# Performance work log

Measured on AMD Instinct MI355X. Metric: run time of the kernel, lower is better.

## Reference

```python
import jax, jax.numpy as jnp
import numpy as np

N_NODES = 2048
N_EDGES = 32768
DIM = 256
HEADS = 4

PARAM_SHAPES = {
    'Wq': (DIM, DIM), 'bq': (DIM,), 'Wk': (DIM, DIM), 'bk': (DIM,),
    'Wv': (DIM, DIM), 'bv': (DIM,), 'Wo': (DIM, DIM), 'bo': (DIM,),
    'gd_W1': (4, 3), 'gd_b1': (3,), 'gd_W2': (3, HEADS), 'gd_b2': (HEADS,),
    'tw_W1': (2 * DIM, DIM), 'tw_b1': (DIM,), 'tw_W2': (DIM, DIM), 'tw_b2': (DIM,),
    'ne_W1': (4 * DIM, 2 * DIM), 'ne_b1': (2 * DIM,), 'ne_W2': (2 * DIM, DIM), 'ne_b2': (DIM,),
    'att_W1': (2 * DIM // HEADS, 2 * DIM // HEADS), 'att_b1': (2 * DIM // HEADS,),
    'att_W2': (DIM // HEADS, 2 * DIM // HEADS), 'att_b2': (DIM // HEADS,),
    'pe_W': (DIM, DIM), 'pe_b': (DIM,), 'pq_W': (DIM, DIM), 'pq_b': (DIM,),
    'pv_W': (DIM, DIM), 'pv_b': (DIM,),
    'pr_W1': (2 * DIM, 2 * DIM), 'pr_b1': (2 * DIM,), 'pr_W2': (2 * DIM, DIM), 'pr_b2': (DIM,),
}


def _lin(x, W, b):
    return x @ W + b


def _mlp2(x, W1, b1, W2, b2):  # Linear-ReLU-Linear (build_mlp, on_last=False)
    return _lin(jnp.maximum(_lin(x, W1, b1), 0.0), W2, b2)


def setup_inputs() -> dict:
    key = jax.random.key(0)
    ks = iter(jax.random.split(key, 64))
    rng = np.random.default_rng(0)
    half = N_EDGES // 2
    s = rng.integers(0, N_NODES, half)
    d = rng.integers(0, N_NODES, half)
    # reciprocal edge pairs so the reverse-edge lookup path is exercised
    edge_index = jnp.asarray(np.stack([np.concatenate([s, d]), np.concatenate([d, s])]), dtype=jnp.int32)
    inp = {
        'node_f': jax.random.normal(next(ks), (N_NODES, DIM), jnp.float32),
        'edge_f': jax.random.normal(next(ks), (N_EDGES, DIM), jnp.float32),
        'coords': jax.random.normal(next(ks), (N_NODES, 3), jnp.float32),
        'edge_index': edge_index,
        'num_heads': HEADS,
    }
    for name, shp in PARAM_SHAPES.items():
        inp[name] = jax.random.normal(next(ks), shp, jnp.float32) * 0.02
    return inp


def _forward(node_f, edge_f, coords, edge_index, num_heads,
             Wq, bq, Wk, bk, Wv, bv, Wo, bo,
             gd_W1, gd_b1, gd_W2, gd_b2,
             tw_W1, tw_b1, tw_W2, tw_b2,
             ne_W1, ne_b1, ne_W2, ne_b2,
             att_W1, att_b1, att_W2, att_b2,
             pe_W, pe_b, pq_W, pq_b, pv_W, pv_b,
             pr_W1, pr_b1, pr_W2, pr_b2):
    N, Dn = node_f.shape
    E, De = edge_f.shape
    H = num_heads
    dh = Wq.shape[1] // H
    src, dst = edge_index[0], edge_index[1]

    # --- NodeUpdate: distance-aware MHSA over all node pairs (batch=1) ---
    q = _lin(node_f, Wq, bq).reshape(N, H, dh)
    k = _lin(node_f, Wk, bk).reshape(N, H, dh)
    v = _lin(node_f, Wv, bv).reshape(N, H, dh)
    diff = coords[:, None, :] - coords[None, :, :]  # [N,N,3]
    sq = jnp.sum(diff * diff, axis=-1, keepdims=True)
    dist = jnp.where(sq > 0, jnp.sqrt(jnp.where(sq > 0, sq, 1.0)), 0.0)
    dmask = _mlp2(jnp.concatenate([diff, dist], -1), gd_W1, gd_b1, gd_W2, gd_b2)  # [N,N,H]
    scores = jnp.einsum('nhd,mhd->hnm', q, k) / float(dh) ** 0.5 + dmask.transpose(2, 0, 1)
    attn = jax.nn.softmax(scores, axis=-1)
    mhsa = _lin(jnp.einsum('hnm,mhd->nhd', attn, v).reshape(N, H * dh), Wo, bo)

    # --- TwinningEdgeAttention: per-node mean of outgoing / incoming edge feats ---
    ones = jnp.ones((E,), edge_f.dtype)
    cnt_s = jnp.maximum(jax.ops.segment_sum(ones, src, num_segments=N), 1.0)
    cnt_d = jnp.maximum(jax.ops.segment_sum(ones, dst, num_segments=N), 1.0)
    sub_mean = jax.ops.segment_sum(edge_f, src, num_segments=N) / cnt_s[:, None]
    obj_mean = jax.ops.segment_sum(edge_f, dst, num_segments=N) / cnt_d[:, None]
    edge_att = jax.nn.sigmoid(_mlp2(jnp.concatenate([sub_mean, obj_mean], -1), tw_W1, tw_b1, tw_W2, tw_b2))
    node_out = jnp.maximum(mhsa, 0.0) * edge_att  # [N, Dn]

    # --- GraphEdgeAttenNetwork ---
    x_i = node_f[src]
    x_j = node_f[dst]
    # reverse-edge matching (vectorized replacement of the python double loop)
    table = jnp.zeros((N * N,), jnp.int32).at[src * N + dst].set(jnp.arange(E, dtype=jnp.int32) + 1)
    rev = table[dst * N + src]
    rev_feat = jnp.where((rev > 0)[:, None], edge_f[jnp.maximum(rev - 1, 0)], 0.0)
    edge_out = _mlp2(jnp.concatenate([x_i, edge_f, rev_feat, x_j], -1), ne_W1, ne_b1, ne_W2, ne_b2)

    value = _lin(x_j, pv_W, pv_b)  # [E, Da]
    query = _lin(x_i, pq_W, pq_b).reshape(E, Dn // H, H)
    edgep = _lin(edge_f, pe_W, pe_b).reshape(E, De // H, H)
    qe = jnp.concatenate([query, edgep], axis=1)  # [E, d_n+d_e, H]
    # conv1d(kernel=1) MLP over channel axis, ReLU between layers
    h = jnp.maximum(jnp.einsum('ech,oc->eoh', qe, att_W1) + att_b1[None, :, None], 0.0)
    prob = jax.nn.softmax(jnp.einsum('ech,oc->eoh', h, att_W2) + att_b2[None, :, None], axis=1)  # [E, d_o, H]
    msg = prob.reshape(E, -1) * value
    agg = jax.ops.segment_max(msg, src, num_segments=N)
    agg = jnp.where(jnp.isfinite(agg), agg, 0.0)  # empty segments -> 0 (torch scatter_max fill)
    xx = _mlp2(jnp.concatenate([node_f, agg], -1), pr_W1, pr_b1, pr_W2, pr_b2)
    return node_out, edge_out, xx


def reference(node_f, edge_f, coords, edge_index, num_heads,
              Wq, bq, Wk, bk, Wv, bv, Wo, bo,
              gd_W1, gd_b1, gd_W2, gd_b2,
              tw_W1, tw_b1, tw_W2, tw_b2,
              ne_W1, ne_b1, ne_W2, ne_b2,
              att_W1, att_b1, att_W2, att_b2,
              pe_W, pe_b, pq_W, pq_b, pv_W, pv_b,
              pr_W1, pr_b1, pr_W2, pr_b2):
    return _forward(node_f, edge_f, coords, edge_index, num_heads,
                    Wq, bq, Wk, bk, Wv, bv, Wo, bo,
                    gd_W1, gd_b1, gd_W2, gd_b2,
                    tw_W1, tw_b1, tw_W2, tw_b2,
                    ne_W1, ne_b1, ne_W2, ne_b2,
                    att_W1, att_b1, att_W2, att_b2,
                    pe_W, pe_b, pq_W, pq_b, pv_W, pv_b,
                    pr_W1, pr_b1, pr_W2, pr_b2)
```

## Files before the change

kernel.cpp:

```cpp
#include <hip/hip_runtime.h>

#define NN 2048
#define NE 32768
#define DIM 256
#define NH 4

typedef unsigned short u16;
typedef __attribute__((ext_vector_type(4))) unsigned short u16x4;
typedef __attribute__((ext_vector_type(8))) short bf16x8;
typedef __attribute__((ext_vector_type(4))) float f32x4;

typedef __attribute__((address_space(1))) const unsigned int g_as1;
typedef __attribute__((address_space(3))) unsigned int l_as3;

__device__ __forceinline__ void gload16(const u16* g, u16* l) {
  __builtin_amdgcn_global_load_lds((g_as1*)g, (l_as3*)l, 16, 0, 0);
}

__device__ __forceinline__ u16 f2bf(float f) {
  unsigned u = __float_as_uint(f);
  unsigned r = u + 0x7FFFu + ((u >> 16) & 1u);
  return (u16)(r >> 16);
}
__device__ __forceinline__ float bf2f(u16 b) {
  return __uint_as_float(((unsigned)b) << 16);
}

struct GB { const u16* A; const int* idx; long ld; long aoffz; };

template<int BNF, int EPI>
__global__ __launch_bounds__(256) void gemm_bf(
    GB ga, const u16* __restrict__ Bt, long bld, long boffz,
    const float* __restrict__ bias, void* __restrict__ Cp, long ldc, long coffz,
    int K, float scale, const float* __restrict__ extra)
{
  __shared__ u16 As[128 * 64];
  __shared__ u16 Bs[32 * BNF * 64];

  const int tid = threadIdx.x;
  const int wid = tid >> 6, lane = tid & 63;
  const int bz = blockIdx.z;
  const int m0 = blockIdx.y * 128;
  const int n0 = blockIdx.x * (32 * BNF);
  const int wr = wid >> 1, wc = wid & 1;
  const int l15 = lane & 15, l4 = lane >> 4;

  const u16* asrc[4];
  #pragma unroll
  for (int c = 0; c < 4; ++c) {
    int rl = c*32 + wid*8 + (lane >> 3);
    int row = ga.idx ? ga.idx[m0 + rl] : (m0 + rl);
    int c16s = (lane & 7) ^ (rl & 7);
    asrc[c] = ga.A + ga.aoffz * bz + (long)row * ga.ld + c16s * 8;
  }
  const u16* bsrc[BNF];
  #pragma unroll
  for (int c = 0; c < BNF; ++c) {
    int rl = c*32 + wid*8 + (lane >> 3);
    int c16s = (lane & 7) ^ (rl & 7);
    bsrc[c] = Bt + boffz * bz + (long)(n0 + rl) * bld + c16s * 8;
  }

  f32x4 acc[4][BNF] = {};

  for (int k0 = 0; k0 < K; k0 += 64) {
    #pragma unroll
    for (int c = 0; c < 4; ++c)
      gload16(asrc[c] + k0, &As[(c*32 + wid*8) * 64]);
    #pragma unroll
    for (int c = 0; c < BNF; ++c)
      gload16(bsrc[c] + k0, &Bs[(c*32 + wid*8) * 64]);
    __syncthreads();

    #pragma unroll
    for (int kk = 0; kk < 2; ++kk) {
      bf16x8 af[4], bfr[BNF];
      #pragma unroll
      for (int i = 0; i < 4; ++i) {
        int r = wr*64 + i*16 + l15;
        af[i] = *(const bf16x8*)&As[r*64 + (((kk*4 + l4) ^ (r & 7)) * 8)];
      }
      #pragma unroll
      for (int j = 0; j < BNF; ++j) {
        int r = wc*(16*BNF) + j*16 + l15;
        bfr[j] = *(const bf16x8*)&Bs[r*64 + (((kk*4 + l4) ^ (r & 7)) * 8)];
      }
      #pragma unroll
      for (int i = 0; i < 4; ++i)
        #pragma unroll
        for (int j = 0; j < BNF; ++j)
          acc[i][j] = __builtin_amdgcn_mfma_f32_16x16x32_bf16(af[i], bfr[j], acc[i][j], 0, 0, 0);
    }
    __syncthreads();
  }

  #pragma unroll
  for (int j = 0; j < BNF; ++j) {
    const int col = n0 + wc*(16*BNF) + j*16 + l15;
    const float bb = bias ? bias[col] : 0.f;
    #pragma unroll
    for (int i = 0; i < 4; ++i) {
      #pragma unroll
      for (int r = 0; r < 4; ++r) {
        const int m = m0 + wr*64 + i*16 + l4*4 + r;
        float v = acc[i][j][r] * scale + bb;
        if constexpr (EPI == 1) v = fmaxf(v, 0.f);
        if constexpr (EPI == 2) v = 1.f / (1.f + expf(-v));
        if constexpr (EPI == 9) {
          v = fmaxf(v, 0.f) * extra[(long)m*ldc + col];
          ((float*)Cp)[(long)m*ldc + col] = v;
        }
        else if constexpr (EPI == 0 || EPI == 2)
          ((float*)Cp)[coffz*bz + (long)m*ldc + col] = v;
        else if constexpr (EPI == 4)
          ((u16*)Cp)[((long)(col & 3) * NE + m) * ldc + (col >> 2) + coffz] = f2bf(v);
        else if constexpr (EPI == 8) {
          if (col < 256)
            ((float*)Cp)[(long)m*256 + (col & 3)*64 + (col >> 2)] = v;
          else {
            u16* qb = (u16*)((float*)Cp + (long)NN*256);
            int c2 = col - 256;
            qb[((long)(c2 & 3)*NN + m)*64 + (c2 >> 2)] = f2bf(v);
          }
        }
        else
          ((u16*)Cp)[coffz*bz + (long)m*ldc + col] = f2bf(v);
      }
    }
  }
}

__global__ __launch_bounds__(256) void flash_k(
    const u16* __restrict__ qkv,
    const u16* __restrict__ vT,
    const float4* __restrict__ pk,
    const float* __restrict__ gW1, const float* __restrict__ gb1,
    const float* __restrict__ gW2, const float* __restrict__ gb2,
    u16* __restrict__ Op,
    float2* __restrict__ ml)
{
  __shared__ u16 Kls[128*64];
  __shared__ u16 Vls[2][64*64];
  __shared__ u16 Pls[4][16*128];

  const int tid = threadIdx.x, wid = tid >> 6, lane = tid & 63;
  const int h  = blockIdx.x & 3;
  const int m0 = (blockIdx.x >> 2) * 64;
  const int part = blockIdx.y;
  const int l15 = lane & 15, l4 = lane >> 4;
  const int rl8 = wid*8 + (lane >> 3);
  const int c8  = lane & 7;

  bf16x8 qf[2];
  {
    const u16* qp = qkv + (long)(m0 + wid*16 + l15)*768 + h*64 + l4*8;
    qf[0] = *(const bf16x8*)(qp);
    qf[1] = *(const bf16x8*)(qp + 32);
  }

  const float b10 = gb1[0], b11 = gb1[1], b12 = gb1[2];
  const float w30 = gW1[9], w31 = gW1[10], w32 = gW1[11];
  const float w20 = gW2[0*4+h], w21 = gW2[1*4+h], w22 = gW2[2*4+h];
  const float b2h = gb2[h];
  float4 rp0[4], rp1[4];
  #pragma unroll
  for (int r = 0; r < 4; ++r) {
    int qrow = m0 + wid*16 + l4*4 + r;
    rp0[r] = pk[qrow*2]; rp1[r] = pk[qrow*2 + 1];
  }

  f32x4 pa[4] = {};
  const int n0 = part*128;

  #pragma unroll
  for (int c = 0; c < 4; ++c) {
    int r = c*32 + rl8;
    gload16(qkv + (long)(n0 + r)*768 + 256 + h*64 + ((c8 ^ (r & 7))*8),
            &Kls[(c*32 + wid*8)*64]);
  }
  #pragma unroll
  for (int hh = 0; hh < 2; ++hh)
    #pragma unroll
    for (int c = 0; c < 2; ++c) {
      int r = c*32 + rl8;
      gload16(vT + (long)(h*64 + r)*NN + n0 + hh*64 + ((c8 ^ (r & 7))*8),
              &Vls[hh][(c*32 + wid*8)*64]);
    }
  __syncthreads();

  f32x4 sa[8] = {};
  #pragma unroll
  for (int kk = 0; kk < 2; ++kk) {
    #pragma unroll
    for (int j = 0; j < 8; ++j) {
      int r = j*16 + l15;
      bf16x8 bf = *(const bf16x8*)&Kls[r*64 + (((kk*4 + l4) ^ (r & 7))*8)];
      sa[j] = __builtin_amdgcn_mfma_f32_16x16x32_bf16(qf[kk], bf, sa[j], 0, 0, 0);
    }
  }

  float rowmx[4] = {-1e30f, -1e30f, -1e30f, -1e30f};
  #pragma unroll
  for (int j = 0; j < 8; ++j) {
    int n = n0 + j*16 + l15;
    float4 cp0 = pk[n*2], cp1 = pk[n*2 + 1];
    #pragma unroll
    for (int r = 0; r < 4; ++r) {
      float dot = rp0[r].x*cp0.x + rp0[r].y*cp0.y + rp0[r].z*cp0.z;
      float sq = rp0[r].w + cp0.w - 2.f*dot;
      float dist = sq > 0.f ? sq * __frsqrt_rn(sq) : 0.f;
      float h0 = fmaxf(b10 + rp1[r].x - cp1.x + dist*w30, 0.f);
      float h1 = fmaxf(b11 + rp1[r].y - cp1.y + dist*w31, 0.f);
      float h2 = fmaxf(b12 + rp1[r].z - cp1.z + dist*w32, 0.f);
      float s = sa[j][r]*0.125f + b2h + h0*w20 + h1*w21 + h2*w22;
      sa[j][r] = s;
      rowmx[r] = fmaxf(rowmx[r], s);
    }
  }
  #pragma unroll
  for (int w = 1; w < 16; w <<= 1)
    #pragma unroll
    for (int r = 0; r < 4; ++r)
      rowmx[r] = fmaxf(rowmx[r], __shfl_xor(rowmx[r], w));

  float rs[4] = {};
  #pragma unroll
  for (int j = 0; j < 8; ++j)
    #pragma unroll
    for (int r = 0; r < 4; ++r) {
      float p = __expf(sa[j][r] - rowmx[r]);
      sa[j][r] = p;
      rs[r] += p;
    }
  #pragma unroll
  for (int w = 1; w < 16; w <<= 1)
    #pragma unroll
    for (int r = 0; r < 4; ++r)
      rs[r] += __shfl_xor(rs[r], w);

  #pragma unroll
  for (int j = 0; j < 8; ++j)
    #pragma unroll
    for (int r = 0; r < 4; ++r) {
      int qr = l4*4 + r, n = j*16 + l15;
      Pls[wid][qr*128 + (((n >> 3) ^ (qr & 7))*8) + (n & 7)] = f2bf(sa[j][r]);
    }
  asm volatile("" ::: "memory");
  #pragma unroll
  for (int ks = 0; ks < 4; ++ks) {
    bf16x8 paf = *(const bf16x8*)&Pls[wid][l15*128 + (((ks*4 + l4) ^ (l15 & 7))*8)];
    #pragma unroll
    for (int j2 = 0; j2 < 4; ++j2) {
      int r = j2*16 + l15;
      bf16x8 vf = *(const bf16x8*)&Vls[ks >> 1][r*64 + ((((ks & 1)*4 + l4) ^ (r & 7))*8)];
      pa[j2] = __builtin_amdgcn_mfma_f32_16x16x32_bf16(paf, vf, pa[j2], 0, 0, 0);
    }
  }

  #pragma unroll
  for (int j2 = 0; j2 < 4; ++j2)
    #pragma unroll
    for (int r = 0; r < 4; ++r) {
      int m = m0 + wid*16 + l4*4 + r;
      Op[((long)part*NN + m)*256 + h*64 + j2*16 + l15] = f2bf(pa[j2][r]);
    }
  if (l15 == 0) {
    #pragma unroll
    for (int r = 0; r < 4; ++r) {
      int m = m0 + wid*16 + l4*4 + r;
      ml[((long)part*NN + m)*4 + h] = make_float2(rowmx[r], rs[r]);
    }
  }
}

__global__ __launch_bounds__(256) void comb_k(const u16* __restrict__ Op,
    const float2* __restrict__ ml, u16* __restrict__ attn) {
  int n = blockIdx.x, t = threadIdx.x, h = t >> 6;
  float m[16], l[16];
  #pragma unroll
  for (int p = 0; p < 16; ++p) { float2 v = ml[((long)p*NN + n)*4 + h]; m[p] = v.x; l[p] = v.y; }
  float M = m[0];
  #pragma unroll
  for (int p = 1; p < 16; ++p) M = fmaxf(M, m[p]);
  float L = 0.f, o = 0.f;
  #pragma unroll
  for (int p = 0; p < 16; ++p) {
    float w = __expf(m[p] - M);
    L += w * l[p];
    o += w * bf2f(Op[((long)p*NN + n)*256 + t]);
  }
  attn[(long)n*256 + t] = f2bf(o / L);
}

__global__ __launch_bounds__(64) void attedge_k(
    const u16* __restrict__ qN, const u16* __restrict__ ep,
    const float* __restrict__ valNp, const int* __restrict__ ei,
    const u16* __restrict__ W1, const float* __restrict__ b1,
    const u16* __restrict__ W2, const float* __restrict__ b2,
    u16* __restrict__ msgP)
{
  __shared__ u16 As[32*128];
  const int lane = threadIdx.x;
  const int h = blockIdx.y;
  const int e0 = blockIdx.x * 32;
  const int l15 = lane & 15, l4 = lane >> 4;

  #pragma unroll
  for (int p = 0; p < 8; ++p) {
    int R0 = p*4;
    int r  = R0 + (lane >> 4);
    int cd = lane & 15;
    int cs = ((cd & 7) ^ (r & 7)) | (cd & 8);
    const u16* src = (cs < 8)
        ? qN + ((long)h*NN + ei[e0 + r])*64 + cs*8
        : ep + ((long)h*NE + e0 + r)*64 + (cs & 7)*8;
    gload16(src, &As[R0*128]);
  }
  __syncthreads();

  f32x4 acc1[2][8] = {};
  #pragma unroll
  for (int kk = 0; kk < 4; ++kk) {
    bf16x8 af[2], bfr[8];
    #pragma unroll
    for (int i = 0; i < 2; ++i) {
      int rA = i*16 + l15;
      int cg = kk*4 + l4;
      int cd = ((cg & 7) ^ (rA & 7)) | (cg & 8);
      af[i] = *(const bf16x8*)&As[rA*128 + cd*8];
    }
    #pragma unroll
    for (int j = 0; j < 8; ++j)
      bfr[j] = *(const bf16x8*)&W1[(long)(j*16 + l15)*128 + kk*32 + l4*8];
    #pragma unroll
    for (int i = 0; i < 2; ++i)
      #pragma unroll
      for (int j = 0; j < 8; ++j)
        acc1[i][j] = __builtin_amdgcn_mfma_f32_16x16x32_bf16(af[i], bfr[j], acc1[i][j], 0, 0, 0);
  }
  __syncthreads();
  #pragma unroll
  for (int i = 0; i < 2; ++i)
    #pragma unroll
    for (int j = 0; j < 8; ++j) {
      int n = j*16 + l15;
      float bb = b1[n];
      #pragma unroll
      for (int r = 0; r < 4; ++r) {
        int m = i*16 + l4*4 + r;
        int cg = n >> 3;
        int cd = ((cg & 7) ^ (m & 7)) | (cg & 8);
        As[m*128 + cd*8 + (n & 7)] = f2bf(fmaxf(acc1[i][j][r] + bb, 0.f));
      }
    }
  __syncthreads();

  f32x4 acc2[2][4] = {};
  #pragma unroll
  for (int kk = 0; kk < 4; ++kk) {
    bf16x8 af[2], bfr[4];
    #pragma unroll
    for (int i = 0; i < 2; ++i) {
      int rA = i*16 + l15;
      int cg = kk*4 + l4;
      int cd = ((cg & 7) ^ (rA & 7)) | (cg & 8);
      af[i] = *(const bf16x8*)&As[rA*128 + cd*8];
    }
    #pragma unroll
    for (int j = 0; j < 4; ++j)
      bfr[j] = *(const bf16x8*)&W2[(long)(j*16 + l15)*128 + kk*32 + l4*8];
    #pragma unroll
    for (int i = 0; i < 2; ++i)
      #pragma unroll
      for (int j = 0; j < 4; ++j)
        acc2[i][j] = __builtin_amdgcn_mfma_f32_16x16x32_bf16(af[i], bfr[j], acc2[i][j], 0, 0, 0);
  }

  #pragma unroll
  for (int i = 0; i < 2; ++i) {
    float mx[4] = {-1e30f,-1e30f,-1e30f,-1e30f};
    #pragma unroll
    for (int j = 0; j < 4; ++j) {
      float bb = b2[j*16 + l15];
      #pragma unroll
      for (int r = 0; r < 4; ++r) {
        acc2[i][j][r] += bb;
        mx[r] = fmaxf(mx[r], acc2[i][j][r]);
      }
    }
    #pragma unroll
    for (int w = 1; w < 16; w <<= 1)
      #pragma unroll
      for (int r = 0; r < 4; ++r) mx[r] = fmaxf(mx[r], __shfl_xor(mx[r], w));
    float sum[4] = {};
    #pragma unroll
    for (int j = 0; j < 4; ++j)
      #pragma unroll
      for (int r = 0; r < 4; ++r) {
        float p = __expf(acc2[i][j][r] - mx[r]);
        acc2[i][j][r] = p; sum[r] += p;
      }
    #pragma unroll
    for (int w = 1; w < 16; w <<= 1)
      #pragma unroll
      for (int r = 0; r < 4; ++r) sum[r] += __shfl_xor(sum[r], w);
    #pragma unroll
    for (int r = 0; r < 4; ++r) {
      int m = i*16 + l4*4 + r;
      int e = e0 + m;
      int dst = ei[NE + e];
      float inv = 1.f / sum[r];
      #pragma unroll
      for (int j = 0; j < 4; ++j) {
        int o = j*16 + l15;
        float v = valNp[(long)dst*256 + h*64 + o];
        msgP[(long)e*256 + h*64 + o] = f2bf(acc2[i][j][r] * inv * v);
      }
    }
  }
}

__global__ __launch_bounds__(512) void gemm_ne(
    const u16* __restrict__ nbf, const u16* __restrict__ ebf, const u16* __restrict__ zbuf,
    const int* __restrict__ ei, const int* __restrict__ rev,
    const u16* __restrict__ Bt, const float* __restrict__ bias, u16* __restrict__ C)
{
  __shared__ u16 As[2][128 * 64];
  __shared__ u16 Bs[2][128 * 64];
  const int tid = threadIdx.x, wid = tid >> 6, lane = tid & 63;
  const int lin = blockIdx.y * 4 + blockIdx.x;
  const int xcd = lin & 7, seq = lin >> 3;
  const int m0 = (xcd*32 + (seq >> 2)) * 128;
  const int n0 = (seq & 3) * 128;
  const int wr = wid >> 2, wc = wid & 3, l15 = lane & 15, l4 = lane >> 4;

  const u16* asrc[4][2];
  #pragma unroll
  for (int c = 0; c < 2; ++c) {
    int rl = c*64 + wid*8 + (lane >> 3);
    int m = m0 + rl;
    int c16s = ((lane & 7) ^ (rl & 7)) * 8;
    int si = ei[m], di = ei[NE + m], rv = rev[m];
    asrc[0][c] = nbf + (long)si * 256 + c16s;
    asrc[1][c] = ebf + (long)m * 256 + c16s;
    asrc[2][c] = (rv >= 0 ? ebf + (long)rv * 256 : zbuf) + c16s;
    asrc[3][c] = nbf + (long)di * 256 + c16s;
  }
  const u16* bsrc[2];
  #pragma unroll
  for (int c = 0; c < 2; ++c) {
    int rl = c*64 + wid*8 + (lane >> 3);
    int c16s = (lane & 7) ^ (rl & 7);
    bsrc[c] = Bt + (long)(n0 + rl) * 1024 + c16s * 8;
  }

  f32x4 acc[4][2] = {};

#define NE_STAGE(BUF, IT) do {                                                  \
    const int seg_ = (IT) >> 2, kt_ = (IT) & 3;                                 \
    _Pragma("unroll")                                                           \
    for (int c = 0; c < 2; ++c)                                                 \
      gload16(asrc[seg_][c] + kt_*64, &As[BUF][(c*64 + wid*8) * 64]);           \
    _Pragma("unroll")                                                           \
    for (int c = 0; c < 2; ++c)                                                 \
      gload16(bsrc[c] + seg_*256 + kt_*64, &Bs[BUF][(c*64 + wid*8) * 64]);      \
  } while (0)

  NE_STAGE(0, 0);
  #pragma unroll
  for (int it = 0; it < 16; ++it) {
    const int b = it & 1;
    if (it < 15) {
      NE_STAGE(b ^ 1, it + 1);
      asm volatile("s_waitcnt vmcnt(4)" ::: "memory");
    } else {
      asm volatile("s_waitcnt vmcnt(0)" ::: "memory");
    }
    __builtin_amdgcn_s_barrier();
    asm volatile("" ::: "memory");
    #pragma unroll
    for (int kk = 0; kk < 2; ++kk) {
      bf16x8 af[4], bfr[2];
      #pragma unroll
      for (int i = 0; i < 4; ++i) {
        int r = wr*64 + i*16 + l15;
        af[i] = *(const bf16x8*)&As[b][r*64 + (((kk*4 + l4) ^ (r & 7)) * 8)];
      }
      #pragma unroll
      for (int j = 0; j < 2; ++j) {
        int r = wc*32 + j*16 + l15;
        bfr[j] = *(const bf16x8*)&Bs[b][r*64 + (((kk*4 + l4) ^ (r & 7)) * 8)];
      }
      #pragma unroll
      for (int i = 0; i < 4; ++i)
        #pragma unroll
        for (int j = 0; j < 2; ++j)
          acc[i][j] = __builtin_amdgcn_mfma_f32_16x16x32_bf16(af[i], bfr[j], acc[i][j], 0, 0, 0);
    }
    asm volatile("" ::: "memory");
    __builtin_amdgcn_s_barrier();
  }
#undef NE_STAGE

  #pragma unroll
  for (int j = 0; j < 2; ++j) {
    const int col = n0 + wc*32 + j*16 + l15;
    const float bb = bias[col];
    #pragma unroll
    for (int i = 0; i < 4; ++i) {
      #pragma unroll
      for (int r = 0; r < 4; ++r) {
        const int m = m0 + wr*64 + i*16 + l4*4 + r;
        C[(long)m*512 + col] = f2bf(fmaxf(acc[i][j][r] + bb, 0.f));
      }
    }
  }
}

struct PrepEnt { const float* src; void* dst; int K; int N; int ntiles; int op; };
struct PrepDesc { PrepEnt e[24]; int n; };

__global__ __launch_bounds__(256) void wprep_k(PrepDesc d) {
  __shared__ float t[32][33];
  int b = blockIdx.x;
  int ei = 0;
  while (ei < d.n && b >= d.e[ei].ntiles) { b -= d.e[ei].ntiles; ++ei; }
  if (ei >= d.n) return;
  PrepEnt E = d.e[ei];
  int tid = threadIdx.x;
  if (E.op == 0) {
    int kt = E.K >> 5;
    int bk = (b % kt) * 32, bn = (b / kt) * 32;
    int tx = tid & 31, ty = tid >> 5;
    #pragma unroll
    for (int i = ty; i < 32; i += 8) t[i][tx] = E.src[(long)(bk + i) * E.N + bn + tx];
    __syncthreads();
    u16* dst = (u16*)E.dst;
    #pragma unroll
    for (int i = ty; i < 32; i += 8) dst[(long)(bn + i) * E.K + bk + tx] = f2bf(t[tx][i]);
  } else if (E.op == 1) {
    long i = (long)b * 256 + tid;
    long n4 = ((long)E.K * E.N) >> 2;
    if (i < n4) {
      float4 v = ((const float4*)E.src)[i];
      u16x4 o = { f2bf(v.x), f2bf(v.y), f2bf(v.z), f2bf(v.w) };
      ((u16x4*)E.dst)[i] = o;
    }
  } else if (E.op == 3) {
    long i = (long)b * 256 + tid;
    long n4 = ((long)E.K * E.N) >> 2;
    if (i < n4) {
      float4 v = ((const float4*)E.src)[i];
      long row = i >> 6;
      long col = (i & 63) * 4;
      u16x4 o = { f2bf(v.x), f2bf(v.y), f2bf(v.z), f2bf(v.w) };
      *(u16x4*)((u16*)E.dst + row*512 + col) = o;
    }
  } else {
    int i = b * 256 + tid;
    if (i < E.N) ((float*)E.dst)[i] = E.src[i];
  }
}

__global__ void geo_k(const float* __restrict__ C3, const float* __restrict__ gW1,
                      float* __restrict__ geo) {
  int n = blockIdx.x * 256 + threadIdx.x;
  if (n >= NN) return;
  float cx = C3[3*n], cy = C3[3*n+1], cz = C3[3*n+2];
  float s = cx*cx + cy*cy + cz*cz;
  float a0 = cx*gW1[0] + cy*gW1[3] + cz*gW1[6];
  float a1 = cx*gW1[1] + cy*gW1[4] + cz*gW1[7];
  float a2 = cx*gW1[2] + cy*gW1[5] + cz*gW1[8];
  float4* g = (float4*)(geo + (long)n*8);
  g[0] = make_float4(cx, cy, cz, s);
  g[1] = make_float4(a0, a1, a2, 0.f);
}

__global__ __launch_bounds__(256) void transb_k(const u16* __restrict__ src,
                                                u16* __restrict__ dst) {
  __shared__ u16 t[32][34];
  int bm = blockIdx.x * 32, bc = blockIdx.y * 32;
  int tx = threadIdx.x & 31, ty = threadIdx.x >> 5;
  #pragma unroll
  for (int i = ty; i < 32; i += 8) t[i][tx] = src[(long)(bm+i)*768 + 512 + bc + tx];
  __syncthreads();
  #pragma unroll
  for (int i = ty; i < 32; i += 8) dst[(long)(bc+i)*NN + bm + tx] = t[tx][i];
}

__global__ void count_k(const int* __restrict__ ei, int* __restrict__ cs,
                        int* __restrict__ cd) {
  int e = blockIdx.x * 256 + threadIdx.x;
  atomicAdd(&cs[ei[e]], 1);
  atomicAdd(&cd[ei[NE + e]], 1);
}

__global__ __launch_bounds__(256) void scan2_k(const int* __restrict__ cnt_all,
    int* __restrict__ start_all, int* __restrict__ cursor_all) {
  const int* cnt = cnt_all + blockIdx.x * NN;
  int* start  = start_all + blockIdx.x * (NN + 1);
  int* cursor = cursor_all + blockIdx.x * NN;
  __shared__ int part[256];
  int t = threadIdx.x;
  int loc[8]; int s = 0;
  #pragma unroll
  for (int i = 0; i < 8; ++i) { int v = cnt[t*8 + i]; loc[i] = s; s += v; }
  part[t] = s;
  __syncthreads();
  if (t == 0) { int a = 0; for (int i = 0; i < 256; ++i) { int v = part[i]; part[i] = a; a += v; } }
  __syncthreads();
  int base = part[t];
  #pragma unroll
  for (int i = 0; i < 8; ++i) { start[t*8+i] = base + loc[i]; cursor[t*8+i] = base + loc[i]; }
  if (t == 255) start[NN] = base + s;
}

__global__ void scatter2_k(const int* __restrict__ ei, int* __restrict__ cur_s,
    int* __restrict__ cur_d, int* __restrict__ eids_s, int* __restrict__ eids_d) {
  int e = blockIdx.x * 256 + threadIdx.x;
  int p = atomicAdd(&cur_s[ei[e]], 1);
  eids_s[p] = e;
  int q = atomicAdd(&cur_d[ei[NE + e]], 1);
  eids_d[q] = e;
}

__global__ void rev2_k(const int* __restrict__ ei, const int* __restrict__ start_s,
    const int* __restrict__ eids_s, int* __restrict__ rev) {
  int e = blockIdx.x * 256 + threadIdx.x;
  int s = ei[e], d = ei[NE + e];
  int b = start_s[d], en = start_s[d+1];
  int best = -1;
  for (int i = b; i < en; ++i) {
    int e2 = eids_s[i];
    if (ei[NE + e2] == s) best = max(best, e2);
  }
  rev[e] = best;
}

__global__ __launch_bounds__(256) void twmean_k(const u16* __restrict__ ebf,
    const int* __restrict__ start_s, const int* __restrict__ eids_s,
    const int* __restrict__ start_d, const int* __restrict__ eids_d,
    u16* __restrict__ twA)
{
  int n = blockIdx.x, t = threadIdx.x, role = blockIdx.y;
  const int* start = role ? start_d : start_s;
  const int* eids  = role ? eids_d  : eids_s;
  int b0 = start[n], e0 = start[n+1];
  float s = 0.f;
  for (int i = b0; i < e0; ++i)
    s += bf2f(ebf[(long)eids[i]*256 + t]);
  twA[(long)n*512 + role*256 + t] = f2bf(s / fmaxf((float)(e0 - b0), 1.f));
}

__global__ __launch_bounds__(256) void agg_k(const int* __restrict__ start,
    const int* __restrict__ eids, const u16* __restrict__ msgP, u16* __restrict__ prA) {
  int n = blockIdx.x, t = threadIdx.x;
  int b = start[n], e_ = start[n+1];
  float mx = -1e30f;
  for (int i = b; i < e_; ++i) {
    int e = eids[i];
    mx = fmaxf(mx, bf2f(msgP[(long)e*256 + t]));
  }
  int c = (t & 63) * 4 + (t >> 6);
  prA[(long)n*512 + 256 + c] = (e_ > b) ? f2bf(mx) : f2bf(0.f);
}

static GB gb(const u16* A, const int* idx, long ld, long aoffz) {
  GB g; g.A = A; g.idx = idx; g.ld = ld; g.aoffz = aoffz; return g;
}

extern "C" void kernel_launch(void* const* d_in, const int* in_sizes, int n_in,
                              void* d_out, int out_size, void* d_ws, size_t ws_size,
                              hipStream_t stream) {
  (void)in_sizes; (void)n_in; (void)out_size; (void)ws_size;

  const float* node_f = (const float*)d_in[0];
  const float* edge_f = (const float*)d_in[1];
  const float* coords = (const float*)d_in[2];
  const int*   ei     = (const int*)d_in[3];
  const float* Wq = (const float*)d_in[5];  const float* bq = (const float*)d_in[6];
  const float* Wk = (const float*)d_in[7];  const float* bk = (const float*)d_in[8];
  const float* Wv = (const float*)d_in[9];  const float* bv = (const float*)d_in[10];
  const float* Wo = (const float*)d_in[11]; const float* bo = (const float*)d_in[12];
  const float* gd_W1 = (const float*)d_in[13]; const float* gd_b1 = (const float*)d_in[14];
  const float* gd_W2 = (const float*)d_in[15]; const float* gd_b2 = (const float*)d_in[16];
  const float* tw_W1 = (const float*)d_in[17]; const float* tw_b1 = (const float*)d_in[18];
  const float* tw_W2 = (const float*)d_in[19]; const float* tw_b2 = (const float*)d_in[20];
  const float* ne_W1 = (const float*)d_in[21]; const float* ne_b1 = (const float*)d_in[22];
  const float* ne_W2 = (const float*)d_in[23]; const float* ne_b2 = (const float*)d_in[24];
  const float* att_W1 = (const float*)d_in[25]; const float* att_b1 = (const float*)d_in[26];
  const float* att_W2 = (const float*)d_in[27]; const float* att_b2 = (const float*)d_in[28];
  const float* pe_W = (const float*)d_in[29]; const float* pe_b = (const float*)d_in[30];
  const float* pq_W = (const float*)d_in[31]; const float* pq_b = (const float*)d_in[32];
  const float* pv_W = (const float*)d_in[33]; const float* pv_b = (const float*)d_in[34];
  const float* pr_W1 = (const float*)d_in[35]; const float* pr_b1 = (const float*)d_in[36];
  const float* pr_W2 = (const float*)d_in[37]; const float* pr_b2 = (const float*)d_in[38];

  char* WB = (char*)d_ws;
  float* out = (float*)d_out;
  float* out_node = out;
  float* out_edge = out + (long)NN*DIM;
  float* out_xx   = out + (long)NN*DIM + (long)NE*DIM;

  const long sz_R1 = 4L*NN*NN*4;
  const long sz_R2 = 4L*NN*NN*2;
  const long sz_R3 = 4L*NE*128*2;
  const long R1 = 0, R2 = R1 + sz_R1, R3 = R2 + sz_R2;

  u16*    Opart = (u16*)(WB + R1);
  float2* mlbuf = (float2*)(WB + R1 + 16L*NN*256*2);
  u16*    msgP  = (u16*)(WB + R1);
  u16*   nehid  = (u16*)(WB + R2);
  u16*   ep     = (u16*)(WB + R3);
  u16*   edge_bf= (u16*)(WB + R3 + (long)NN*NN*4);

  long cur = R3 + sz_R3;
  auto alloc = [&](long bytes) { long o = cur; cur += (bytes + 255) & ~255L; return o; };

  long o_sub = alloc((long)NN*768*2 + (long)NN*DIM*2 + (long)NN*DIM*2);
  u16* qkv_bf  = (u16*)(WB + o_sub);
  u16* vT      = qkv_bf + (long)NN*768;
  u16* attn_bf = vT + (long)NN*DIM;

  long o_cs  = alloc(2L*NN*4);
  int* cs_i = (int*)(WB + o_cs); int* cd_i = cs_i + NN;
  long o_ea  = alloc((long)NN*DIM*4);  float* eatt = (float*)(WB + o_ea);
  long o_rv  = alloc((long)NE*4);      int* rev = (int*)(WB + o_rv);
  long o_st  = alloc(2L*(NN+1)*4);     int* start_s = (int*)(WB + o_st);
  int* start_d = start_s + (NN + 1);
  long o_cu  = alloc(2L*NN*4);         int* cursor_s = (int*)(WB + o_cu);
  int* cursor_d = cursor_s + NN;
  long o_eid = alloc(2L*NE*4);         int* eids_s = (int*)(WB + o_eid);
  int* eids_d = eids_s + NE;
  long o_zb  = alloc(1024);            u16* zbuf = (u16*)(WB + o_zb);
  long o_geo = alloc((long)NN*8*4);    float* geo = (float*)(WB + o_geo);
  long o_nbf = alloc((long)NN*DIM*2);  u16* node_bf = (u16*)(WB + o_nbf);
  long o_twA = alloc((long)NN*512*2);  u16* twA = (u16*)(WB + o_twA);
  long o_twh = alloc((long)NN*DIM*2);  u16* twh = (u16*)(WB + o_twh);
  long o_prA = alloc((long)NN*512*2);  u16* prA = (u16*)(WB + o_prA);
  long o_prh = alloc((long)NN*512*2);  u16* prh = (u16*)(WB + o_prh);
  long o_vN  = alloc((long)NN*256*4 + 4L*NN*64*2);
  float* valN = (float*)(WB + o_vN);
  u16*   qN   = (u16*)(valN + (long)NN*256);

  u16* qkv_t = (u16*)(WB + alloc(3L*DIM*DIM*2));
  u16* Wo_t  = (u16*)(WB + alloc(DIM*DIM*2));
  u16* tw1_t = (u16*)(WB + alloc(DIM*512*2));
  u16* tw2_t = (u16*)(WB + alloc(DIM*DIM*2));
  u16* ne1_t = (u16*)(WB + alloc(512L*1024*2));
  u16* ne2_t = (u16*)(WB + alloc(DIM*512*2));
  u16* pe_t  = (u16*)(WB + alloc(DIM*DIM*2));
  u16* pvq_t = (u16*)(WB + alloc(2L*DIM*DIM*2));
  u16* pr1_t = (u16*)(WB + alloc(512L*512*2));
  u16* pr2_t = (u16*)(WB + alloc(DIM*512*2));
  u16* a1_bf = (u16*)(WB + alloc(128*128*2));
  u16* a2_bf = (u16*)(WB + alloc(64*128*2));
  float* qkvb = (float*)(WB + alloc(768*4));
  float* pvqb = (float*)(WB + alloc(512*4));

  hipMemsetAsync(cs_i, 0, 2L*NN*4, stream);
  hipMemsetAsync(zbuf, 0, 1024, stream);

  PrepDesc pd{}; int ne_ = 0; int tot = 0;
  auto addT = [&](const float* s, u16* d, int K, int N) {
    pd.e[ne_] = { s, d, K, N, (K/32)*(N/32), 0 }; tot += pd.e[ne_].ntiles; ++ne_;
  };
  auto addC = [&](const float* s, u16* d, long elems) {
    int nt = (int)((elems/4 + 255) / 256);
    pd.e[ne_] = { s, d, 1, (int)elems, nt, 1 }; tot += nt; ++ne_;
  };
  auto addB = [&](const float* s, float* d, int n) {
    pd.e[ne_] = { s, d, 1, n, (n + 255)/256, 2 }; tot += pd.e[ne_].ntiles; ++ne_;
  };
  addT(Wq, qkv_t,               DIM, DIM);
  addT(Wk, qkv_t + DIM*DIM,     DIM, DIM);
  addT(Wv, qkv_t + 2*DIM*DIM,   DIM, DIM);
  addT(Wo, Wo_t, DIM, DIM);
  addT(tw_W1, tw1_t, 512, DIM);
  addT(tw_W2, tw2_t, DIM, DIM);
  addT(ne_W1, ne1_t, 1024, 512);
  addT(ne_W2, ne2_t, 512, DIM);
  addT(pe_W, pe_t, DIM, DIM);
  addT(pv_W, pvq_t,             DIM, DIM);
  addT(pq_W, pvq_t + DIM*DIM,   DIM, DIM);
  addT(pr_W1, pr1_t, 512, 512);
  addT(pr_W2, pr2_t, 512, DIM);
  addC(att_W1, a1_bf, 128*128);
  addC(att_W2, a2_bf, 64*128);
  addC(node_f, node_bf, (long)NN*DIM);
  addC(edge_f, edge_bf, (long)NE*DIM);
  addB(bq, qkvb, 256); addB(bk, qkvb + 256, 256); addB(bv, qkvb + 512, 256);
  addB(pv_b, pvqb, 256); addB(pq_b, pvqb + 256, 256);
  pd.e[ne_] = { node_f, prA, NN, 256, (int)(((long)NN*256/4 + 255)/256), 3 };
  tot += pd.e[ne_].ntiles; ++ne_;
  pd.n = ne_;
  wprep_k<<<tot, 256, 0, stream>>>(pd);
  geo_k<<<NN/256, 256, 0, stream>>>(coords, gd_W1, geo);

  count_k<<<NE/256, 256, 0, stream>>>(ei, cs_i, cd_i);
  scan2_k<<<2, 256, 0, stream>>>(cs_i, start_s, cursor_s);
  scatter2_k<<<NE/256, 256, 0, stream>>>(ei, cursor_s, cursor_d, eids_s, eids_d);
  rev2_k<<<NE/256, 256, 0, stream>>>(ei, start_s, eids_s, rev);
  twmean_k<<<dim3(NN,2), 256, 0, stream>>>(edge_bf, start_s, eids_s, start_d, eids_d, twA);
  gemm_bf<4,1><<<dim3(2,16,1), 256, 0, stream>>>(gb(twA, nullptr, 512, 0), tw1_t, 512, 0,
      tw_b1, twh, DIM, 0, 512, 1.f, nullptr);
  gemm_bf<4,2><<<dim3(2,16,1), 256, 0, stream>>>(gb(twh, nullptr, DIM, 0), tw2_t, DIM, 0,
      tw_b2, eatt, DIM, 0, DIM, 1.f, nullptr);

  gemm_bf<4,5><<<dim3(6,16,1), 256, 0, stream>>>(gb(node_bf, nullptr, DIM, 0), qkv_t, DIM, 0,
      qkvb, qkv_bf, 768, 0, DIM, 1.f, nullptr);
  transb_k<<<dim3(64,8), 256, 0, stream>>>(qkv_bf, vT);
  flash_k<<<dim3(128,16), 256, 0, stream>>>(qkv_bf, vT, (const float4*)geo,
      gd_W1, gd_b1, gd_W2, gd_b2, Opart, mlbuf);
  comb_k<<<NN, 256, 0, stream>>>(Opart, mlbuf, attn_bf);
  gemm_bf<4,9><<<dim3(2,16,1), 256, 0, stream>>>(gb(attn_bf, nullptr, DIM, 0), Wo_t, DIM, 0,
      bo, out_node, DIM, 0, DIM, 1.f, eatt);

  gemm_ne<<<dim3(4,256,1), 512, 0, stream>>>(node_bf, edge_bf, zbuf, ei, rev,
      ne1_t, ne_b1, nehid);
  gemm_bf<4,0><<<dim3(2,256,1), 256, 0, stream>>>(gb(nehid, nullptr, 512, 0), ne2_t, 512, 0,
      ne_b2, out_edge, DIM, 0, 512, 1.f, nullptr);

  gemm_bf<4,8><<<dim3(4,16,1), 256, 0, stream>>>(gb(node_bf, nullptr, DIM, 0), pvq_t, DIM, 0,
      pvqb, valN, 256, 0, DIM, 1.f, nullptr);
  gemm_bf<4,4><<<dim3(2,256,1), 256, 0, stream>>>(gb(edge_bf, nullptr, DIM, 0), pe_t, DIM, 0,
      pe_b, ep, 64, 0, DIM, 1.f, nullptr);
  attedge_k<<<dim3(NE/32, NH), 64, 0, stream>>>(qN, ep, valN, ei,
      a1_bf, att_b1, a2_bf, att_b2, msgP);
  agg_k<<<NN, 256, 0, stream>>>(start_s, eids_s, msgP, prA);

  gemm_bf<4,1><<<dim3(4,16,1), 256, 0, stream>>>(gb(prA, nullptr, 512, 0), pr1_t, 512, 0,
      pr_b1, prh, 512, 0, 512, 1.f, nullptr);
  gemm_bf<4,0><<<dim3(2,16,1), 256, 0, stream>>>(gb(prh, nullptr, 512, 0), pr2_t, 512, 0,
      pr_b2, out_xx, DIM, 0, 512, 1.f, nullptr);
}
```

Before: 377.6 us.

## Process edges in source-sorted order and alias flash P buffer onto K LDS

The edge-attention kernel now walks edges in source-sorted order via eids_s and writes messages at sorted positions, so the segment-max aggregation reads contiguous rows instead of gathering by edge id. Separately, the flash attention kernel reuses the K shared-memory tile for the P staging buffer after a barrier, cutting LDS per block so more blocks can be resident. The cost is an extra index indirection on the attedge loads and one added __syncthreads in flash_k.

```diff
diff --git a/kernel.cpp b/kernel.cpp
--- a/kernel.cpp
+++ b/kernel.cpp
@@ -139,9 +139,8 @@
     u16* __restrict__ Op,
     float2* __restrict__ ml)
 {
-  __shared__ u16 Kls[128*64];
+  __shared__ u16 KP[128*64];
   __shared__ u16 Vls[2][64*64];
-  __shared__ u16 Pls[4][16*128];
 
   const int tid = threadIdx.x, wid = tid >> 6, lane = tid & 63;
   const int h  = blockIdx.x & 3;
@@ -176,7 +175,7 @@
   for (int c = 0; c < 4; ++c) {
     int r = c*32 + rl8;
     gload16(qkv + (long)(n0 + r)*768 + 256 + h*64 + ((c8 ^ (r & 7))*8),
-            &Kls[(c*32 + wid*8)*64]);
+            &KP[(c*32 + wid*8)*64]);
   }
   #pragma unroll
   for (int hh = 0; hh < 2; ++hh)
@@ -194,7 +193,7 @@
     #pragma unroll
     for (int j = 0; j < 8; ++j) {
       int r = j*16 + l15;
-      bf16x8 bf = *(const bf16x8*)&Kls[r*64 + (((kk*4 + l4) ^ (r & 7))*8)];
+      bf16x8 bf = *(const bf16x8*)&KP[r*64 + (((kk*4 + l4) ^ (r & 7))*8)];
       sa[j] = __builtin_amdgcn_mfma_f32_16x16x32_bf16(qf[kk], bf, sa[j], 0, 0, 0);
     }
   }
@@ -238,22 +237,26 @@
     for (int r = 0; r < 4; ++r)
       rs[r] += __shfl_xor(rs[r], w);
 
-  #pragma unroll
-  for (int j = 0; j < 8; ++j)
-    #pragma unroll
-    for (int r = 0; r < 4; ++r) {
-      int qr = l4*4 + r, n = j*16 + l15;
-      Pls[wid][qr*128 + (((n >> 3) ^ (qr & 7))*8) + (n & 7)] = f2bf(sa[j][r]);
-    }
-  asm volatile("" ::: "memory");
-  #pragma unroll
-  for (int ks = 0; ks < 4; ++ks) {
-    bf16x8 paf = *(const bf16x8*)&Pls[wid][l15*128 + (((ks*4 + l4) ^ (l15 & 7))*8)];
-    #pragma unroll
-    for (int j2 = 0; j2 < 4; ++j2) {
-      int r = j2*16 + l15;
-      bf16x8 vf = *(const bf16x8*)&Vls[ks >> 1][r*64 + ((((ks & 1)*4 + l4) ^ (r & 7))*8)];
-      pa[j2] = __builtin_amdgcn_mfma_f32_16x16x32_bf16(paf, vf, pa[j2], 0, 0, 0);
+  __syncthreads();
+  {
+    u16* Pw = &KP[wid * 16 * 128];
+    #pragma unroll
+    for (int j = 0; j < 8; ++j)
+      #pragma unroll
+      for (int r = 0; r < 4; ++r) {
+        int qr = l4*4 + r, n = j*16 + l15;
+        Pw[qr*128 + (((n >> 3) ^ (qr & 7))*8) + (n & 7)] = f2bf(sa[j][r]);
+      }
+    asm volatile("" ::: "memory");
+    #pragma unroll
+    for (int ks = 0; ks < 4; ++ks) {
+      bf16x8 paf = *(const bf16x8*)&Pw[l15*128 + (((ks*4 + l4) ^ (l15 & 7))*8)];
+      #pragma unroll
+      for (int j2 = 0; j2 < 4; ++j2) {
+        int r = j2*16 + l15;
+        bf16x8 vf = *(const bf16x8*)&Vls[ks >> 1][r*64 + ((((ks & 1)*4 + l4) ^ (r & 7))*8)];
+        pa[j2] = __builtin_amdgcn_mfma_f32_16x16x32_bf16(paf, vf, pa[j2], 0, 0, 0);
+      }
     }
   }
 
@@ -295,6 +298,7 @@
 __global__ __launch_bounds__(64) void attedge_k(
     const u16* __restrict__ qN, const u16* __restrict__ ep,
     const float* __restrict__ valNp, const int* __restrict__ ei,
+    const int* __restrict__ eids_s,
     const u16* __restrict__ W1, const float* __restrict__ b1,
     const u16* __restrict__ W2, const float* __restrict__ b2,
     u16* __restrict__ msgP)
@@ -309,11 +313,12 @@
   for (int p = 0; p < 8; ++p) {
     int R0 = p*4;
     int r  = R0 + (lane >> 4);
+    int eid = eids_s[e0 + r];
     int cd = lane & 15;
     int cs = ((cd & 7) ^ (r & 7)) | (cd & 8);
     const u16* src = (cs < 8)
-        ? qN + ((long)h*NN + ei[e0 + r])*64 + cs*8
-        : ep + ((long)h*NE + e0 + r)*64 + (cs & 7)*8;
+        ? qN + ((long)h*NN + ei[eid])*64 + cs*8
+        : ep + ((long)h*NE + eid)*64 + (cs & 7)*8;
     gload16(src, &As[R0*128]);
   }
   __syncthreads();
@@ -407,14 +412,15 @@
     #pragma unroll
     for (int r = 0; r < 4; ++r) {
       int m = i*16 + l4*4 + r;
-      int e = e0 + m;
-      int dst = ei[NE + e];
+      int pos = e0 + m;
+      int eid = eids_s[pos];
+      int dst = ei[NE + eid];
       float inv = 1.f / sum[r];
       #pragma unroll
       for (int j = 0; j < 4; ++j) {
         int o = j*16 + l15;
         float v = valNp[(long)dst*256 + h*64 + o];
-        msgP[(long)e*256 + h*64 + o] = f2bf(acc2[i][j][r] * inv * v);
+        msgP[(long)pos*256 + h*64 + o] = f2bf(acc2[i][j][r] * inv * v);
       }
     }
   }
@@ -653,14 +659,12 @@
 }
 
 __global__ __launch_bounds__(256) void agg_k(const int* __restrict__ start,
-    const int* __restrict__ eids, const u16* __restrict__ msgP, u16* __restrict__ prA) {
+    const u16* __restrict__ msgP, u16* __restrict__ prA) {
   int n = blockIdx.x, t = threadIdx.x;
   int b = start[n], e_ = start[n+1];
   float mx = -1e30f;
-  for (int i = b; i < e_; ++i) {
-    int e = eids[i];
-    mx = fmaxf(mx, bf2f(msgP[(long)e*256 + t]));
-  }
+  for (int i = b; i < e_; ++i)
+    mx = fmaxf(mx, bf2f(msgP[(long)i*256 + t]));
   int c = (t & 63) * 4 + (t >> 6);
   prA[(long)n*512 + 256 + c] = (e_ > b) ? f2bf(mx) : f2bf(0.f);
 }
@@ -825,9 +829,9 @@
       pvqb, valN, 256, 0, DIM, 1.f, nullptr);
   gemm_bf<4,4><<<dim3(2,256,1), 256, 0, stream>>>(gb(edge_bf, nullptr, DIM, 0), pe_t, DIM, 0,
       pe_b, ep, 64, 0, DIM, 1.f, nullptr);
-  attedge_k<<<dim3(NE/32, NH), 64, 0, stream>>>(qN, ep, valN, ei,
+  attedge_k<<<dim3(NE/32, NH), 64, 0, stream>>>(qN, ep, valN, ei, eids_s,
       a1_bf, att_b1, a2_bf, att_b2, msgP);
-  agg_k<<<NN, 256, 0, stream>>>(start_s, eids_s, msgP, prA);
+  agg_k<<<NN, 256, 0, stream>>>(start_s, msgP, prA);
 
   gemm_bf<4,1><<<dim3(4,16,1), 256, 0, stream>>>(gb(prA, nullptr, 512, 0), pr1_t, 512, 0,
       pr_b1, prh, 512, 0, 512, 1.f, nullptr);
```

After: 379.8 us. No clear change (+0.6%).
